# Kernel tuning notes

Measured on AMD Instinct MI355X. Metric: run time of the kernel, lower is better.

Reference implementation:

```python
import jax, jax.numpy as jnp
import numpy as np

# BCQLinear packed forward: weight[o, i] reconstructed from per-(out,group,bit)
# alpha scales and +/-1 binary codes via einsum('oib,oiab->oia'), then a plain
# out-channel-wise matmul (in_ch_wise=False) plus bias. beta is NOT used in the
# packed forward path of the original module.

B, S = 2, 1024          # token dims (m...)
O = 4096                 # out_features
G, A, NB = 32, 128, 3    # n_groups, group_size, n_bits; in_features = G*A = 4096


def setup_inputs() -> dict:
    key = jax.random.key(0)
    k1, k2, k3, k4 = jax.random.split(key, 4)
    x = jax.random.normal(k1, (B, S, G * A), dtype=jnp.float32)
    # binary codes are strictly +/-1 (Packer.unpack yields sign bits)
    b = jnp.sign(jax.random.normal(k2, (O, G, A, NB)))
    binary = jnp.where(b == 0, 1.0, b).astype(jnp.float32)
    # alpha scales are small positive magnitudes in practice
    alpha = jax.random.uniform(k3, (O, G, NB), dtype=jnp.float32,
                               minval=0.01, maxval=0.1)
    bias = 0.01 * jax.random.normal(k4, (O,), dtype=jnp.float32)
    return {"input": x, "binary": binary, "alpha": alpha, "bias": bias}


def reference(input, binary, alpha, bias):
    # dequantize: [O, G, A] -> [O, I]
    weight = jnp.einsum('oib,oiab->oia', alpha, binary).reshape(binary.shape[0], -1)
    # out-channel-wise matmul: m...i, oi -> m...o
    out = jnp.einsum('msi,oi->mso', input, weight) + bias
    return out
```

## Files before the change

kernel.cpp:

```cpp
#include <hip/hip_runtime.h>
#include <hip/hip_bf16.h>
#include <stdint.h>

typedef __bf16 bf16x8 __attribute__((ext_vector_type(8)));
typedef __bf16 bf16x4 __attribute__((ext_vector_type(4)));
typedef float  f32x4  __attribute__((ext_vector_type(4)));

static constexpr int Mdim = 2048;
static constexpr int Ndim = 4096;
static constexpr int Kdim = 4096;

__global__ __launch_bounds__(256)
void bcq_dequant(const float* __restrict__ binary, const float* __restrict__ alpha,
                 __bf16* __restrict__ w) {
  long t = (long)blockIdx.x * blockDim.x + threadIdx.x;
  long e = t * 4;
  if (e >= (long)Ndim * Kdim) return;
  int o = (int)(e >> 12);
  int i = (int)(e & 4095);
  int g = i >> 7;
  const float* al = alpha + ((long)o * 32 + g) * 3;
  float a0 = al[0], a1 = al[1], a2 = al[2];
  const float4* bs = (const float4*)(binary + e * 3);
  float4 b0 = bs[0], b1 = bs[1], b2 = bs[2];
  bf16x4 wv;
  wv[0] = (__bf16)(a0 * b0.x + a1 * b0.y + a2 * b0.z);
  wv[1] = (__bf16)(a0 * b0.w + a1 * b1.x + a2 * b1.y);
  wv[2] = (__bf16)(a0 * b1.z + a1 * b1.w + a2 * b2.x);
  wv[3] = (__bf16)(a0 * b2.y + a1 * b2.z + a2 * b2.w);
  *(bf16x4*)(w + e) = wv;
}

__global__ __launch_bounds__(256)
void cvt_bf16(const float* __restrict__ x, __bf16* __restrict__ xb, long n) {
  long t = (long)blockIdx.x * blockDim.x + threadIdx.x;
  long e = t * 8;
  if (e >= n) return;
  float4 v0 = *(const float4*)(x + e);
  float4 v1 = *(const float4*)(x + e + 4);
  bf16x8 r;
  r[0] = (__bf16)v0.x; r[1] = (__bf16)v0.y; r[2] = (__bf16)v0.z; r[3] = (__bf16)v0.w;
  r[4] = (__bf16)v1.x; r[5] = (__bf16)v1.y; r[6] = (__bf16)v1.z; r[7] = (__bf16)v1.w;
  *(bf16x8*)(xb + e) = r;
}

#define BM 128
#define BN 128
#define BK 32

__device__ static inline void g2l16(const void* g, void* l) {
  __builtin_amdgcn_global_load_lds(
      (const __attribute__((address_space(1))) void*)g,
      (__attribute__((address_space(3))) void*)l, 16, 0, 0);
}

__global__ __launch_bounds__(256, 2)
void gemm_bt(const __bf16* __restrict__ A, const __bf16* __restrict__ Bw,
             const float* __restrict__ bias, float* __restrict__ C) {
  __shared__ __bf16 sA[BM * BK];
  __shared__ __bf16 sB[BN * BK];
  const int tid  = threadIdx.x;
  const int lane = tid & 63;
  const int wave = tid >> 6;
  const int wm = wave >> 1, wn = wave & 1;
  const int bm = blockIdx.x & 15;
  const int bn = blockIdx.x >> 4;
  const int m0 = bm * BM, n0 = bn * BN;

  f32x4 acc[4][4] = {};

  const int lr = lane & 15;
  const int kk = (lane >> 4) * 8;

  const int r0 = tid >> 2;
  const int c0 = (tid & 3) * 8;
  const __bf16* Ab = A  + (long)(m0 + r0) * Kdim + c0;
  const __bf16* Bb = Bw + (long)(n0 + r0) * Kdim + c0;

  for (int k0 = 0; k0 < Kdim; k0 += BK) {
    g2l16(Ab,             sA + wave * 512);
    g2l16(Ab + 64 * Kdim, sA + 2048 + wave * 512);
    g2l16(Bb,             sB + wave * 512);
    g2l16(Bb + 64 * Kdim, sB + 2048 + wave * 512);
    Ab += BK; Bb += BK;
    __syncthreads();

    bf16x8 afrag[4], bfrag[4];
#pragma unroll
    for (int f = 0; f < 4; ++f) {
      afrag[f] = *(const bf16x8*)(sA + (wm * 64 + f * 16 + lr) * BK + kk);
      bfrag[f] = *(const bf16x8*)(sB + (wn * 64 + f * 16 + lr) * BK + kk);
    }
#pragma unroll
    for (int mf = 0; mf < 4; ++mf)
#pragma unroll
      for (int nf = 0; nf < 4; ++nf)
        acc[mf][nf] = __builtin_amdgcn_mfma_f32_16x16x32_bf16(
            afrag[mf], bfrag[nf], acc[mf][nf], 0, 0, 0);
    __syncthreads();
  }

#pragma unroll
  for (int nf = 0; nf < 4; ++nf) {
    const int gcol = n0 + wn * 64 + nf * 16 + lr;
    const float bv = bias[gcol];
#pragma unroll
    for (int mf = 0; mf < 4; ++mf) {
#pragma unroll
      for (int r = 0; r < 4; ++r) {
        const int grow = m0 + wm * 64 + mf * 16 + (lane >> 4) * 4 + r;
        C[(long)grow * Ndim + gcol] = acc[mf][nf][r] + bv;
      }
    }
  }
}

extern "C" void kernel_launch(void* const* d_in, const int* in_sizes, int n_in,
                              void* d_out, int out_size, void* d_ws, size_t ws_size,
                              hipStream_t stream) {
  const float* x      = (const float*)d_in[0];
  const float* binary = (const float*)d_in[1];
  const float* alpha  = (const float*)d_in[2];
  const float* bias   = (const float*)d_in[3];
  float* out = (float*)d_out;

  __bf16* wb = (__bf16*)d_ws;
  __bf16* xb = wb + (size_t)Ndim * Kdim;

  {
    long n4 = (long)Ndim * Kdim / 4;
    bcq_dequant<<<(int)((n4 + 255) / 256), 256, 0, stream>>>(binary, alpha, wb);
  }
  {
    long n8 = (long)Mdim * Kdim / 8;
    cvt_bf16<<<(int)((n8 + 255) / 256), 256, 0, stream>>>(x, xb, (long)Mdim * Kdim);
  }
  gemm_bt<<<dim3((Mdim / BM) * (Ndim / BN)), 256, 0, stream>>>(xb, wb, bias, out);
}
```

Measured before the change: 138.4 us.

## Replace GEMM with 256x256 split-K pipelined MFMA kernel plus reduction

```diff
diff --git a/kernel.cpp b/kernel.cpp
--- a/kernel.cpp
+++ b/kernel.cpp
@@ -44,75 +44,171 @@
   *(bf16x8*)(xb + e) = r;
 }
 
-#define BM 128
-#define BN 128
-#define BK 32
-
-__device__ static inline void g2l16(const void* g, void* l) {
+__global__ __launch_bounds__(256)
+void reduce_add(const float* __restrict__ p0, const float* __restrict__ p1,
+                const float* __restrict__ bias, float* __restrict__ out) {
+  long e = ((long)blockIdx.x * 256 + threadIdx.x) * 4;
+  if (e >= (long)Mdim * Ndim) return;
+  float4 a = *(const float4*)(p0 + e);
+  float4 b = *(const float4*)(p1 + e);
+  int col = (int)(e & (Ndim - 1));
+  float4 bv = *(const float4*)(bias + col);
+  float4 r;
+  r.x = a.x + b.x + bv.x; r.y = a.y + b.y + bv.y;
+  r.z = a.z + b.z + bv.z; r.w = a.w + b.w + bv.w;
+  *(float4*)(out + e) = r;
+}
+
+static constexpr int BK = 64;
+static constexpr int KSLICE = 2048;
+static constexpr int NT = KSLICE / BK;
+static constexpr int ITERS = NT / 2;
+
+__device__ __forceinline__ void g2l16(const void* g, void* l) {
   __builtin_amdgcn_global_load_lds(
       (const __attribute__((address_space(1))) void*)g,
       (__attribute__((address_space(3))) void*)l, 16, 0, 0);
 }
 
-__global__ __launch_bounds__(256, 2)
-void gemm_bt(const __bf16* __restrict__ A, const __bf16* __restrict__ Bw,
-             const float* __restrict__ bias, float* __restrict__ C) {
-  __shared__ __bf16 sA[BM * BK];
-  __shared__ __bf16 sB[BN * BK];
-  const int tid  = threadIdx.x;
-  const int lane = tid & 63;
-  const int wave = tid >> 6;
-  const int wm = wave >> 1, wn = wave & 1;
-  const int bm = blockIdx.x & 15;
-  const int bn = blockIdx.x >> 4;
-  const int m0 = bm * BM, n0 = bn * BN;
-
-  f32x4 acc[4][4] = {};
-
-  const int lr = lane & 15;
-  const int kk = (lane >> 4) * 8;
-
-  const int r0 = tid >> 2;
-  const int c0 = (tid & 3) * 8;
-  const __bf16* Ab = A  + (long)(m0 + r0) * Kdim + c0;
-  const __bf16* Bb = Bw + (long)(n0 + r0) * Kdim + c0;
-
-  for (int k0 = 0; k0 < Kdim; k0 += BK) {
-    g2l16(Ab,             sA + wave * 512);
-    g2l16(Ab + 64 * Kdim, sA + 2048 + wave * 512);
-    g2l16(Bb,             sB + wave * 512);
-    g2l16(Bb + 64 * Kdim, sB + 2048 + wave * 512);
-    Ab += BK; Bb += BK;
-    __syncthreads();
-
-    bf16x8 afrag[4], bfrag[4];
-#pragma unroll
-    for (int f = 0; f < 4; ++f) {
-      afrag[f] = *(const bf16x8*)(sA + (wm * 64 + f * 16 + lr) * BK + kk);
-      bfrag[f] = *(const bf16x8*)(sB + (wn * 64 + f * 16 + lr) * BK + kk);
-    }
-#pragma unroll
-    for (int mf = 0; mf < 4; ++mf)
-#pragma unroll
-      for (int nf = 0; nf < 4; ++nf)
-        acc[mf][nf] = __builtin_amdgcn_mfma_f32_16x16x32_bf16(
-            afrag[mf], bfrag[nf], acc[mf][nf], 0, 0, 0);
-    __syncthreads();
-  }
-
-#pragma unroll
-  for (int nf = 0; nf < 4; ++nf) {
-    const int gcol = n0 + wn * 64 + nf * 16 + lr;
-    const float bv = bias[gcol];
-#pragma unroll
-    for (int mf = 0; mf < 4; ++mf) {
+#define BAR()    __builtin_amdgcn_s_barrier()
+#define LGKM0()  asm volatile("s_waitcnt lgkmcnt(0)" ::: "memory")
+#define SCHED0() __builtin_amdgcn_sched_barrier(0)
+
+#define STAGE_A(t, H, b) do { \
+  _Pragma("unroll") for (int j_ = 0; j_ < 2; ++j_) \
+    g2l16(baseA[j_] + (H) * 128 * Kdim + (t) * 64, \
+          sm + (b) * 65536 + (H) * 16384 + (w * 2 + j_) * 1024); \
+} while (0)
+#define STAGE_B(t, H, b) do { \
+  _Pragma("unroll") for (int j_ = 0; j_ < 2; ++j_) \
+    g2l16(baseB[j_] + (H) * 128 * Kdim + (t) * 64, \
+          sm + (b) * 65536 + 32768 + (H) * 16384 + (w * 2 + j_) * 1024); \
+} while (0)
+
+#define LOAD_A4(dst, b, m0_) do { \
+  _Pragma("unroll") for (int m_ = 0; m_ < 4; ++m_) \
+    _Pragma("unroll") for (int h_ = 0; h_ < 2; ++h_) \
+      dst[m_][h_] = *(const bf16x8*)(sm + (b) * 65536 + aoffbase + ((m0_) + m_) * 2048 + swz[h_]); \
+} while (0)
+#define LOAD_B2(dst, b, n0_) do { \
+  _Pragma("unroll") for (int n_ = 0; n_ < 2; ++n_) \
+    _Pragma("unroll") for (int h_ = 0; h_ < 2; ++h_) \
+      dst[n_][h_] = *(const bf16x8*)(sm + (b) * 65536 + boffbase + ((n0_) + n_) * 2048 + swz[h_]); \
+} while (0)
+
+#define MMA8(fa_, fb_, m0_, n0_) do { \
+  __builtin_amdgcn_s_setprio(1); \
+  _Pragma("unroll") for (int m_ = 0; m_ < 4; ++m_) \
+    _Pragma("unroll") for (int n_ = 0; n_ < 2; ++n_) { \
+      acc[(m0_) + m_][(n0_) + n_] = __builtin_amdgcn_mfma_f32_16x16x32_bf16( \
+          fa_[m_][0], fb_[n_][0], acc[(m0_) + m_][(n0_) + n_], 0, 0, 0); \
+      acc[(m0_) + m_][(n0_) + n_] = __builtin_amdgcn_mfma_f32_16x16x32_bf16( \
+          fa_[m_][1], fb_[n_][1], acc[(m0_) + m_][(n0_) + n_], 0, 0, 0); \
+    } \
+  __builtin_amdgcn_s_setprio(0); \
+} while (0)
+
+__global__ __launch_bounds__(512, 2)
+void gemm8(const __bf16* __restrict__ A, const __bf16* __restrict__ Bw,
+           float* __restrict__ P) {
+  __shared__ __align__(128) char sm[131072];
+  const int tid = threadIdx.x, lane = tid & 63, w = tid >> 6;
+  const int wm = w >> 2, wn = w & 3;
+
+  const int bid = blockIdx.x;
+  const int logical = (bid & 7) * 32 + (bid >> 3);
+  const int ks = logical >> 7;
+  const int tile = logical & 127;
+  const int tm = tile & 7, tn = tile >> 3;
+  const int kbase = ks * KSLICE;
+
+  float* Pout = P + (long)ks * Mdim * Ndim;
+
+  const int rlo = lane >> 3;
+  const int gsw = (lane & 7) ^ rlo;
+  const __bf16* baseA[2];
+  const __bf16* baseB[2];
+#pragma unroll
+  for (int j = 0; j < 2; ++j) {
+    int rp = (w * 2 + j) * 8 + rlo;
+    baseA[j] = A  + (long)(tm * 256 + rp) * Kdim + kbase + gsw * 8;
+    baseB[j] = Bw + (long)(tn * 256 + rp) * Kdim + kbase + gsw * 8;
+  }
+
+  int swz[2];
+#pragma unroll
+  for (int h = 0; h < 2; ++h)
+    swz[h] = (((h * 4 + (lane >> 4)) ^ (lane & 7)) << 4);
+  const int aoffbase = (wm * 128 + (lane & 15)) * 128;
+  const int boffbase = 32768 + (wn * 64 + (lane & 15)) * 128;
+
+  f32x4 acc[8][4] = {};
+
+  STAGE_A(0, 0, 0); STAGE_A(0, 1, 0); STAGE_B(0, 0, 0); STAGE_B(0, 1, 0);
+  STAGE_B(1, 0, 1); STAGE_B(1, 1, 1);
+  asm volatile("s_waitcnt vmcnt(4)" ::: "memory");
+  BAR();
+
+  bf16x8 fa[4][2], fb01[2][2], fb23[2][2];
+
+  for (int i = 0; i < ITERS; ++i) {
+    const int t0 = 2 * i, t1 = 2 * i + 1;
+    const bool pf = (i < ITERS - 1);
+    LOAD_A4(fa, 0, 0); LOAD_B2(fb01, 0, 0);
+    STAGE_A(t1, 0, 1);
+    BAR(); LGKM0(); SCHED0();
+    MMA8(fa, fb01, 0, 0);
+    BAR();
+    LOAD_B2(fb23, 0, 2);
+    STAGE_A(t1, 1, 1);
+    BAR(); LGKM0(); SCHED0();
+    MMA8(fa, fb23, 0, 2);
+    BAR();
+    LOAD_A4(fa, 0, 4);
+    if (pf) STAGE_B(t0 + 2, 0, 0);
+    BAR(); LGKM0(); SCHED0();
+    MMA8(fa, fb01, 4, 0);
+    BAR();
+    if (pf) STAGE_B(t0 + 2, 1, 0);
+    if (i == ITERS - 1) { asm volatile("s_waitcnt vmcnt(0)" ::: "memory"); }
+    else                { asm volatile("s_waitcnt vmcnt(4)" ::: "memory"); }
+    BAR();
+    MMA8(fa, fb23, 4, 2);
+    BAR();
+    LOAD_A4(fa, 1, 0); LOAD_B2(fb01, 1, 0);
+    if (pf) STAGE_A(t0 + 2, 0, 0);
+    BAR(); LGKM0(); SCHED0();
+    MMA8(fa, fb01, 0, 0);
+    BAR();
+    LOAD_B2(fb23, 1, 2);
+    if (pf) STAGE_A(t0 + 2, 1, 0);
+    BAR(); LGKM0(); SCHED0();
+    MMA8(fa, fb23, 0, 2);
+    BAR();
+    LOAD_A4(fa, 1, 4);
+    if (pf) STAGE_B(t1 + 2, 0, 1);
+    BAR(); LGKM0(); SCHED0();
+    MMA8(fa, fb01, 4, 0);
+    BAR();
+    if (pf) STAGE_B(t1 + 2, 1, 1);
+    asm volatile("s_waitcnt vmcnt(4)" ::: "memory");
+    BAR();
+    MMA8(fa, fb23, 4, 2);
+    BAR();
+  }
+
+  const int r4 = (lane >> 4) * 4;
+  const int cl = lane & 15;
+#pragma unroll
+  for (int m = 0; m < 8; ++m)
+#pragma unroll
+    for (int n = 0; n < 4; ++n)
 #pragma unroll
       for (int r = 0; r < 4; ++r) {
-        const int grow = m0 + wm * 64 + mf * 16 + (lane >> 4) * 4 + r;
-        C[(long)grow * Ndim + gcol] = acc[mf][nf][r] + bv;
+        int row = tm * 256 + wm * 128 + m * 16 + r4 + r;
+        int col = tn * 256 + wn * 64 + n * 16 + cl;
+        Pout[(long)row * Ndim + col] = acc[m][n][r];
       }
-    }
-  }
 }
 
 extern "C" void kernel_launch(void* const* d_in, const int* in_sizes, int n_in,
@@ -126,6 +222,7 @@
 
   __bf16* wb = (__bf16*)d_ws;
   __bf16* xb = wb + (size_t)Ndim * Kdim;
+  float*  pp = (float*)(xb + (size_t)Mdim * Kdim);
 
   {
     long n4 = (long)Ndim * Kdim / 4;
@@ -135,5 +232,10 @@
     long n8 = (long)Mdim * Kdim / 8;
     cvt_bf16<<<(int)((n8 + 255) / 256), 256, 0, stream>>>(x, xb, (long)Mdim * Kdim);
   }
-  gemm_bt<<<dim3((Mdim / BM) * (Ndim / BN)), 256, 0, stream>>>(xb, wb, bias, out);
-}
+  gemm8<<<dim3(256), 512, 0, stream>>>(xb, wb, pp);
+  {
+    long n4 = (long)Mdim * Ndim / 4;
+    reduce_add<<<(int)((n4 + 255) / 256), 256, 0, stream>>>(
+        pp, pp + (size_t)Mdim * Ndim, bias, out);
+  }
+}
```

Measured after the change: 133.8 us. 3.3% less time.
